# Kernel tuning notes

Measured on AMD Instinct MI355X. Metric: run time of the kernel, lower is better.

The kernel has to match this reference:

```python
import jax, jax.numpy as jnp
import numpy as np

N_NODES = 100000
N_FEAT = 256
HIDDEN = 16
N_CLASSES = 16
N_EDGES = 3200000


def setup_inputs() -> dict:
    key = jax.random.key(0)
    k = jax.random.split(key, 7)
    x = jax.random.normal(k[0], (N_NODES, N_FEAT), dtype=jnp.float32)
    edge_index = jax.random.randint(k[1], (2, N_EDGES), 0, N_NODES, dtype=jnp.int32)
    # GCNConv: linear (no bias) + bias added after aggregation
    s1 = 1.0 / np.sqrt(N_FEAT)
    W1 = jax.random.uniform(k[2], (N_FEAT, HIDDEN), jnp.float32, -s1, s1)
    b1 = jnp.zeros((HIDDEN,), jnp.float32)
    # SAGEConv: lin_l (on aggregated neighbors, with bias) + lin_r (root)
    s2 = 1.0 / np.sqrt(HIDDEN)
    Wl = jax.random.uniform(k[3], (HIDDEN, N_CLASSES), jnp.float32, -s2, s2)
    Wr = jax.random.uniform(k[4], (HIDDEN, N_CLASSES), jnp.float32, -s2, s2)
    b2 = jax.random.uniform(k[5], (N_CLASSES,), jnp.float32, -s2, s2)
    return {"x": x, "edge_index": edge_index, "W1": W1, "b1": b1,
            "Wl": Wl, "Wr": Wr, "b2": b2}


def reference(x, edge_index, W1, b1, Wl, Wr, b2):
    N = x.shape[0]
    src, dst = edge_index[0], edge_index[1]

    # ---- GCNConv(num_features -> hidden): transform, add self-loops,
    # symmetric normalization, sum-aggregate, add bias ----
    h = x @ W1  # [N, H]
    loop = jnp.arange(N, dtype=src.dtype)
    src2 = jnp.concatenate([src, loop])
    dst2 = jnp.concatenate([dst, loop])
    ones = jnp.ones(src2.shape[0], dtype=h.dtype)
    deg = jax.ops.segment_sum(ones, dst2, num_segments=N)  # in-degree incl. self-loop
    dinv = jnp.where(deg > 0, jax.lax.rsqrt(deg), 0.0)
    norm = dinv[src2] * dinv[dst2]  # [E+N]
    msgs = h[src2] * norm[:, None]
    h1 = jax.ops.segment_sum(msgs, dst2, num_segments=N) + b1  # [N, H]

    # ---- SAGEConv(hidden -> num_classes, aggr='mean') ----
    cnt = jax.ops.segment_sum(jnp.ones(src.shape[0], dtype=h1.dtype), dst, num_segments=N)
    agg = jax.ops.segment_sum(h1[src], dst, num_segments=N)
    agg = agg / jnp.maximum(cnt, 1.0)[:, None]  # mean over neighbors
    out = agg @ Wl + h1 @ Wr + b2  # [N, C]

    return jax.nn.log_softmax(out, axis=1)
```

## Files before the change

### kernel.cpp

```cpp
#include <hip/hip_runtime.h>
#include <cstddef>

#define NF 256
#define NH 16
#define NC 16

#define BN    128
#define BSH   7
#define BMSK  127
#define CAP   4608
#define AVLEN 16
#define ACH   (256*AVLEN)
#define NBMAX 800

typedef __attribute__((ext_vector_type(8))) short bf16x8;
typedef __attribute__((ext_vector_type(4))) float f32x4;

__device__ inline short f2bf(float f) {
    union { float f; unsigned int u; } v; v.f = f;
    const unsigned int r = v.u + 0x7FFFu + ((v.u >> 16) & 1u);
    return (short)(r >> 16);
}
__device__ inline float bf2f(unsigned short u) {
    union { unsigned int i; float f; } v; v.i = ((unsigned int)u) << 16;
    return v.f;
}

__global__ __launch_bounds__(256) void fusedAG_kernel(
    const int* __restrict__ src, const int* __restrict__ dst,
    unsigned int* __restrict__ bfill, unsigned int* __restrict__ bpairs,
    const float* __restrict__ x, const float* __restrict__ W1,
    float* __restrict__ hs_u, int E, int NBK, int NCH, int N)
{
    __shared__ unsigned int hist[NBMAX];
    __shared__ unsigned int sbase[NBMAX];
    __shared__ unsigned int gpos[NBMAX];
    __shared__ unsigned int tmp[1024];
    __shared__ unsigned int reorder[ACH];
    __shared__ unsigned short wbid[ACH];

    const int tid = threadIdx.x;

    if (blockIdx.x < (unsigned)NCH) {
        for (int i = tid; i < NBMAX; i += 256) hist[i] = 0u;
        __syncthreads();

        const int base = blockIdx.x * ACH;
        unsigned int pv[AVLEN];
        unsigned int ps[AVLEN];
        #pragma unroll
        for (int l = 0; l < AVLEN; ++l) {
            const int e = base + l * 256 + tid;
            if (e < E) {
                const unsigned int s = (unsigned int)src[e];
                const unsigned int d = (unsigned int)dst[e];
                const unsigned int b = d >> BSH;
                pv[l] = (s << BSH) | (d & BMSK);
                const unsigned int slot = atomicAdd(&hist[b], 1u);
                ps[l] = (slot << 10) | b;
            } else {
                ps[l] = 0xFFFFFFFFu;
            }
        }
        __syncthreads();

        for (int i = tid; i < 1024; i += 256) tmp[i] = (i < NBK) ? hist[i] : 0u;
        __syncthreads();
        for (int off = 1; off < 1024; off <<= 1) {
            unsigned int v0 = 0, v1 = 0, v2 = 0, v3 = 0;
            const int i0 = tid, i1 = tid + 256, i2 = tid + 512, i3 = tid + 768;
            if (i0 >= off) v0 = tmp[i0 - off];
            if (i1 >= off) v1 = tmp[i1 - off];
            if (i2 >= off) v2 = tmp[i2 - off];
            if (i3 >= off) v3 = tmp[i3 - off];
            __syncthreads();
            tmp[i0] += v0; tmp[i1] += v1; tmp[i2] += v2; tmp[i3] += v3;
            __syncthreads();
        }
        for (int i = tid; i < NBK; i += 256) {
            const unsigned int h = hist[i];
            sbase[i] = tmp[i] - h;
            if (h) gpos[i] = atomicAdd(&bfill[i], h);
        }
        const int cc = (base + ACH <= E) ? ACH : (E - base);
        __syncthreads();

        #pragma unroll
        for (int l = 0; l < AVLEN; ++l) {
            if (ps[l] != 0xFFFFFFFFu) {
                const unsigned int b = ps[l] & 1023u;
                const unsigned int i = sbase[b] + (ps[l] >> 10);
                reorder[i] = pv[l];
                wbid[i] = (unsigned short)b;
            }
        }
        __syncthreads();

        for (int i = tid; i < cc; i += 256) {
            const unsigned int b = wbid[i];
            const unsigned int g = gpos[b] + ((unsigned int)i - sbase[b]);
            if (g < CAP) bpairs[(size_t)b * CAP + g] = reorder[i];
        }
    } else {
        const int gb = blockIdx.x - NCH;
        const int lane = tid & 63;
        const int wave = tid >> 6;
        const int quad = lane >> 4;
        const int mn   = lane & 15;

        bf16x8 bfrag[8];
        #pragma unroll
        for (int kc = 0; kc < 8; ++kc) {
            #pragma unroll
            for (int j = 0; j < 8; ++j) {
                const int k = kc * 32 + quad * 8 + j;
                bfrag[kc][j] = f2bf(W1[k * NH + mn]);
            }
        }

        #pragma unroll
        for (int t = 0; t < 2; ++t) {
            const int tile = gb * 8 + wave * 2 + t;
            const int n0 = tile * 16;
            if (n0 >= N) break;

            f32x4 acc = {0.f, 0.f, 0.f, 0.f};
            const float* xrow = x + (size_t)(n0 + mn) * NF + quad * 8;
            #pragma unroll
            for (int kc = 0; kc < 8; ++kc) {
                const float4 lo = *(const float4*)(xrow + kc * 32);
                const float4 hi = *(const float4*)(xrow + kc * 32 + 4);
                bf16x8 af;
                af[0] = f2bf(lo.x); af[1] = f2bf(lo.y); af[2] = f2bf(lo.z); af[3] = f2bf(lo.w);
                af[4] = f2bf(hi.x); af[5] = f2bf(hi.y); af[6] = f2bf(hi.z); af[7] = f2bf(hi.w);
                acc = __builtin_amdgcn_mfma_f32_16x16x32_bf16(af, bfrag[kc], acc, 0, 0, 0);
            }

            #pragma unroll
            for (int r = 0; r < 4; ++r) {
                const int row = quad * 4 + r;
                hs_u[(size_t)(n0 + row) * NH + mn] = acc[r];
            }
        }
    }
}

__global__ __launch_bounds__(256) void bucketB_kernel(
    const unsigned int* __restrict__ bfill, unsigned int* __restrict__ bpairs,
    const float* __restrict__ hs_u,
    int* __restrict__ rowptr, int* __restrict__ cnt, float* __restrict__ dinv,
    unsigned short* __restrict__ hs_bf, int N)
{
    __shared__ unsigned int pairs[CAP];
    __shared__ unsigned int ssorted[CAP];
    __shared__ unsigned int hist[BN];
    __shared__ unsigned int scan[BN];
    __shared__ unsigned int cursor[BN];
    __shared__ float sdinv[BN];

    const int tid = threadIdx.x;
    const int b = blockIdx.x;
    const size_t bbase = (size_t)b * CAP;
    const int nodeBase = b * BN;
    unsigned int m = bfill[b]; if (m > CAP) m = CAP;

    if (tid < BN) hist[tid] = 0u;
    __syncthreads();

    for (unsigned int i = tid; i < m; i += 256) {
        const unsigned int p = bpairs[bbase + i];
        pairs[i] = p;
        atomicAdd(&hist[p & BMSK], 1u);
    }
    __syncthreads();

    if (tid < BN) scan[tid] = hist[tid];
    __syncthreads();
    for (int off = 1; off < BN; off <<= 1) {
        unsigned int v = 0;
        if (tid < BN && tid >= off) v = scan[tid - off];
        __syncthreads();
        if (tid < BN) scan[tid] += v;
        __syncthreads();
    }
    if (tid < BN) cursor[tid] = scan[tid] - hist[tid];
    __syncthreads();

    for (unsigned int i = tid; i < m; i += 256) {
        const unsigned int p = pairs[i];
        const unsigned int pos = atomicAdd(&cursor[p & BMSK], 1u);
        ssorted[pos] = p >> BSH;
    }
    __syncthreads();

    for (unsigned int i = tid; i < m; i += 256)
        bpairs[bbase + i] = ssorted[i];

    if (tid < BN) {
        const int n = nodeBase + tid;
        const unsigned int h = hist[tid];
        const float dv = rsqrtf((float)h + 1.0f);
        sdinv[tid] = dv;
        if (n < N) {
            cnt[n] = (int)h;
            dinv[n] = dv;
            rowptr[n] = (int)(b * CAP + (scan[tid] - h));
        }
    }
    __syncthreads();

    for (int t = tid; t < BN * NH; t += 256) {
        const int n = nodeBase + (t >> 4);
        if (n < N) {
            const size_t idx = (size_t)n * NH + (t & 15);
            hs_bf[idx] = (unsigned short)f2bf(hs_u[idx] * sdinv[t >> 4]);
        }
    }
}

__global__ __launch_bounds__(256) void gcn_gather_kernel(
    const unsigned short* __restrict__ hs_bf, const unsigned int* __restrict__ csrc,
    const int* __restrict__ rowptr, const int* __restrict__ cnt,
    const float* __restrict__ dinv, const float* __restrict__ b1,
    unsigned short* __restrict__ h1_bf, int N)
{
    const int tid = threadIdx.x;
    const int n = blockIdx.x * 16 + (tid >> 4);
    if (n >= N) return;
    const int j = tid & 15;
    const int start = rowptr[n];
    const int end = start + cnt[n];

    float acc = bf2f(hs_bf[(size_t)n * NH + j]);
    int k = start;
    for (; k + 16 <= end; k += 16) {
        const int myi = (int)csrc[k + j];
        float s = 0.f;
        #pragma unroll
        for (int u = 0; u < 16; ++u) {
            const int sidx = __shfl(myi, u, 16);
            s += bf2f(hs_bf[(size_t)sidx * NH + j]);
        }
        acc += s;
    }
    for (; k < end; ++k)
        acc += bf2f(hs_bf[(size_t)csrc[k] * NH + j]);

    h1_bf[(size_t)n * NH + j] = (unsigned short)f2bf(b1[j] + dinv[n] * acc);
}

__global__ __launch_bounds__(256) void sage_out_kernel(
    const unsigned short* __restrict__ h1_bf, const unsigned int* __restrict__ csrc,
    const int* __restrict__ rowptr, const int* __restrict__ cnt,
    const float* __restrict__ Wl, const float* __restrict__ Wr,
    const float* __restrict__ b2, float* __restrict__ out, int N)
{
    __shared__ float wls[NH * NC];
    __shared__ float wrs[NH * NC];
    __shared__ float b2s[NC];
    const int tid = threadIdx.x;
    if (tid < NH * NC) { wls[tid] = Wl[tid]; wrs[tid] = Wr[tid]; }
    if (tid < NC) b2s[tid] = b2[tid];
    __syncthreads();

    const int n = blockIdx.x * 16 + (tid >> 4);
    if (n >= N) return;
    const int j = tid & 15;
    const int start = rowptr[n];
    const int deg = cnt[n];
    const int end = start + deg;

    float acc = 0.f;
    int k = start;
    for (; k + 16 <= end; k += 16) {
        const int myi = (int)csrc[k + j];
        float s = 0.f;
        #pragma unroll
        for (int u = 0; u < 16; ++u) {
            const int sidx = __shfl(myi, u, 16);
            s += bf2f(h1_bf[(size_t)sidx * NH + j]);
        }
        acc += s;
    }
    for (; k < end; ++k)
        acc += bf2f(h1_bf[(size_t)csrc[k] * NH + j]);

    const float aggj = acc / fmaxf((float)deg, 1.0f);
    const float h1j  = bf2f(h1_bf[(size_t)n * NH + j]);

    float o = b2s[j];
    #pragma unroll
    for (int kk = 0; kk < NH; ++kk) {
        const float a  = __shfl(aggj, kk, 16);
        const float hh = __shfl(h1j,  kk, 16);
        o += a * wls[kk * NC + j] + hh * wrs[kk * NC + j];
    }

    float m = o;
    #pragma unroll
    for (int off = 1; off < 16; off <<= 1) m = fmaxf(m, __shfl_xor(m, off, 16));
    const float ex = expf(o - m);
    float ssum = ex;
    #pragma unroll
    for (int off = 1; off < 16; off <<= 1) ssum += __shfl_xor(ssum, off, 16);

    out[(size_t)n * NC + j] = (o - m) - logf(ssum);
}

extern "C" void kernel_launch(void* const* d_in, const int* in_sizes, int n_in,
                              void* d_out, int out_size, void* d_ws, size_t ws_size,
                              hipStream_t stream)
{
    const float* x  = (const float*)d_in[0];
    const int*   ei = (const int*)d_in[1];
    const float* W1 = (const float*)d_in[2];
    const float* b1 = (const float*)d_in[3];
    const float* Wl = (const float*)d_in[4];
    const float* Wr = (const float*)d_in[5];
    const float* b2 = (const float*)d_in[6];
    float* out = (float*)d_out;

    const int N = in_sizes[0] / NF;
    const int E = in_sizes[1] / 2;
    const int* src = ei;
    const int* dst = ei + E;

    const int NBK = (N + BN - 1) / BN;
    const int NCH = (E + ACH - 1) / ACH;
    const int tiles = (N + 15) / 16;
    const int GEMMB = (tiles + 7) / 8;

    unsigned short* hs_bf = (unsigned short*)d_ws;
    unsigned short* h1_bf = hs_bf + (size_t)N * NH;
    float* hs_u   = (float*)(h1_bf + (size_t)N * NH);
    float* dinv   = hs_u + (size_t)N * NH;
    int*   cnt    = (int*)(dinv + N);
    int*   rowptr = cnt + N;
    unsigned int* bfill  = (unsigned int*)(rowptr + N);
    unsigned int* bpairs = bfill + 1024;

    hipMemsetAsync(bfill, 0, (size_t)NBK * sizeof(unsigned int), stream);

    fusedAG_kernel<<<NCH + GEMMB, 256, 0, stream>>>(
        src, dst, bfill, bpairs, x, W1, hs_u, E, NBK, NCH, N);
    bucketB_kernel<<<NBK, 256, 0, stream>>>(
        bfill, bpairs, hs_u, rowptr, cnt, dinv, hs_bf, N);

    const int nodeBlk = (N + 15) / 16;
    gcn_gather_kernel<<<nodeBlk, 256, 0, stream>>>(hs_bf, bpairs, rowptr, cnt, dinv, b1, h1_bf, N);
    sage_out_kernel<<<nodeBlk, 256, 0, stream>>>(h1_bf, bpairs, rowptr, cnt, Wl, Wr, b2, out, N);
}
```

Measured before the change: 316.0 us.

## Interleave scatter and GEMM blocks; vectorize gather tail with masked shuffle loop

In the fused first kernel, block IDs now alternate between edge-bucketing work and MFMA GEMM tiles instead of putting all bucketing blocks first. This lets memory-bound scatter and compute-bound GEMM blocks run side by side on each CU. Both gather kernels also replace the serial per-edge remainder loop with one masked 16-wide shuffle iteration. That removes the scalar, latency-bound tail at the cost of a few redundant loads of a clamped index.

```diff
diff --git a/kernel.cpp b/kernel.cpp
--- a/kernel.cpp
+++ b/kernel.cpp
@@ -30,7 +30,7 @@
     const int* __restrict__ src, const int* __restrict__ dst,
     unsigned int* __restrict__ bfill, unsigned int* __restrict__ bpairs,
     const float* __restrict__ x, const float* __restrict__ W1,
-    float* __restrict__ hs_u, int E, int NBK, int NCH, int N)
+    float* __restrict__ hs_u, int E, int NBK, int NCH, int GEMMB, int N)
 {
     __shared__ unsigned int hist[NBMAX];
     __shared__ unsigned int sbase[NBMAX];
@@ -41,11 +41,21 @@
 
     const int tid = threadIdx.x;
 
-    if (blockIdx.x < (unsigned)NCH) {
+    const int nInter = 2 * (NCH < GEMMB ? NCH : GEMMB);
+    int msId = -1, gbId = -1;
+    const int bi = (int)blockIdx.x;
+    if (bi < nInter) {
+        if (bi & 1) gbId = bi >> 1; else msId = bi >> 1;
+    } else {
+        const int r = bi - nInter;
+        if (NCH > GEMMB) msId = (nInter >> 1) + r; else gbId = (nInter >> 1) + r;
+    }
+
+    if (msId >= 0) {
         for (int i = tid; i < NBMAX; i += 256) hist[i] = 0u;
         __syncthreads();
 
-        const int base = blockIdx.x * ACH;
+        const int base = msId * ACH;
         unsigned int pv[AVLEN];
         unsigned int ps[AVLEN];
         #pragma unroll
@@ -102,7 +112,6 @@
             if (g < CAP) bpairs[(size_t)b * CAP + g] = reorder[i];
         }
     } else {
-        const int gb = blockIdx.x - NCH;
         const int lane = tid & 63;
         const int wave = tid >> 6;
         const int quad = lane >> 4;
@@ -120,7 +129,7 @@
 
         #pragma unroll
         for (int t = 0; t < 2; ++t) {
-            const int tile = gb * 8 + wave * 2 + t;
+            const int tile = gbId * 8 + wave * 2 + t;
             const int n0 = tile * 16;
             if (n0 >= N) break;
 
@@ -232,19 +241,29 @@
     const int end = start + cnt[n];
 
     float acc = bf2f(hs_bf[(size_t)n * NH + j]);
-    int k = start;
-    for (; k + 16 <= end; k += 16) {
-        const int myi = (int)csrc[k + j];
-        float s = 0.f;
-        #pragma unroll
-        for (int u = 0; u < 16; ++u) {
-            const int sidx = __shfl(myi, u, 16);
-            s += bf2f(hs_bf[(size_t)sidx * NH + j]);
-        }
-        acc += s;
-    }
-    for (; k < end; ++k)
-        acc += bf2f(hs_bf[(size_t)csrc[k] * NH + j]);
+    for (int k = start; k < end; k += 16) {
+        const int idx = k + j;
+        const int myi = (int)csrc[idx < end ? idx : (end - 1)];
+        const int rem = end - k;
+        if (rem >= 16) {
+            float s = 0.f;
+            #pragma unroll
+            for (int u = 0; u < 16; ++u) {
+                const int sidx = __shfl(myi, u, 16);
+                s += bf2f(hs_bf[(size_t)sidx * NH + j]);
+            }
+            acc += s;
+        } else {
+            float s = 0.f;
+            #pragma unroll
+            for (int u = 0; u < 16; ++u) {
+                const int sidx = __shfl(myi, u, 16);
+                const float v = bf2f(hs_bf[(size_t)sidx * NH + j]);
+                s += (u < rem) ? v : 0.f;
+            }
+            acc += s;
+        }
+    }
 
     h1_bf[(size_t)n * NH + j] = (unsigned short)f2bf(b1[j] + dinv[n] * acc);
 }
@@ -271,19 +290,29 @@
     const int end = start + deg;
 
     float acc = 0.f;
-    int k = start;
-    for (; k + 16 <= end; k += 16) {
-        const int myi = (int)csrc[k + j];
-        float s = 0.f;
-        #pragma unroll
-        for (int u = 0; u < 16; ++u) {
-            const int sidx = __shfl(myi, u, 16);
-            s += bf2f(h1_bf[(size_t)sidx * NH + j]);
-        }
-        acc += s;
-    }
-    for (; k < end; ++k)
-        acc += bf2f(h1_bf[(size_t)csrc[k] * NH + j]);
+    for (int k = start; k < end; k += 16) {
+        const int idx = k + j;
+        const int myi = (int)csrc[idx < end ? idx : (end - 1)];
+        const int rem = end - k;
+        if (rem >= 16) {
+            float s = 0.f;
+            #pragma unroll
+            for (int u = 0; u < 16; ++u) {
+                const int sidx = __shfl(myi, u, 16);
+                s += bf2f(h1_bf[(size_t)sidx * NH + j]);
+            }
+            acc += s;
+        } else {
+            float s = 0.f;
+            #pragma unroll
+            for (int u = 0; u < 16; ++u) {
+                const int sidx = __shfl(myi, u, 16);
+                const float v = bf2f(h1_bf[(size_t)sidx * NH + j]);
+                s += (u < rem) ? v : 0.f;
+            }
+            acc += s;
+        }
+    }
 
     const float aggj = acc / fmaxf((float)deg, 1.0f);
     const float h1j  = bf2f(h1_bf[(size_t)n * NH + j]);
@@ -342,7 +371,7 @@
     hipMemsetAsync(bfill, 0, (size_t)NBK * sizeof(unsigned int), stream);
 
     fusedAG_kernel<<<NCH + GEMMB, 256, 0, stream>>>(
-        src, dst, bfill, bpairs, x, W1, hs_u, E, NBK, NCH, N);
+        src, dst, bfill, bpairs, x, W1, hs_u, E, NBK, NCH, GEMMB, N);
     bucketB_kernel<<<NBK, 256, 0, stream>>>(
         bfill, bpairs, hs_u, rowptr, cnt, dinv, hs_bf, N);
 
```

Measured after the change: 278.5 us. 1.13x faster.
